# Performance work log

Hardware: AMD Instinct MI355X
Metric: run time of the kernel (lower is better)

The kernel has to match this reference:

```python
import jax, jax.numpy as jnp
import numpy as np

N_NODES = 20000
N_EDGES = 640000
NUM_TYPES = 100
D = 512


def sage_layer(h, src, dst, Ws, Wn, b):
    # DGL SAGEConv(aggregator='mean'): mean over in-neighbors (messages flow src->dst)
    msg = jax.ops.segment_sum(h[src], dst, num_segments=N_NODES)  # [N, d]
    deg = jax.ops.segment_sum(jnp.ones((src.shape[0],), h.dtype), dst, num_segments=N_NODES)
    h_neigh = msg / jnp.maximum(deg, 1.0)[:, None]
    return h @ Ws + h_neigh @ Wn + b


def setup_inputs() -> dict:
    key = jax.random.key(0)
    ks = jax.random.split(key, 10)
    s = 1.0 / np.sqrt(D)
    return {
        "in_feat": jax.random.randint(ks[0], (N_NODES,), 0, NUM_TYPES),
        "src": jax.random.randint(ks[1], (N_EDGES,), 0, N_NODES),
        "dst": jax.random.randint(ks[2], (N_EDGES,), 0, N_NODES),
        "emb": jax.random.normal(ks[3], (NUM_TYPES, D), dtype=jnp.float32),
        "Ws0": jax.random.normal(ks[4], (D, D), dtype=jnp.float32) * s,
        "Wn0": jax.random.normal(ks[5], (D, D), dtype=jnp.float32) * s,
        "b0": jnp.zeros((D,), jnp.float32),
        "Ws1": jax.random.normal(ks[6], (D, D), dtype=jnp.float32) * s,
        "Wn1": jax.random.normal(ks[7], (D, D), dtype=jnp.float32) * s,
        "b1": jnp.zeros((D,), jnp.float32),
    }


def reference(in_feat, src, dst, emb, Ws0, Wn0, b0, Ws1, Wn1, b1):
    h = emb[in_feat]                                   # embedding lookup [N, D]
    h = jax.nn.relu(sage_layer(h, src, dst, Ws0, Wn0, b0))
    h = jax.nn.relu(sage_layer(h, src, dst, Ws1, Wn1, b1))
    return h
```

## Files before the change

### kernel.cpp

```cpp
#include <hip/hip_runtime.h>
#include <hip/hip_bf16.h>
#include <stdint.h>

#define N_NODES 20000
#define N_EDGES 640000
#define DIM     512
#define M_PAD   20096
#define NTYPE   100
#define KEXT    256
#define CSTRIDE 96
#define CURS    16

using bf16 = __hip_bfloat16;
typedef __attribute__((ext_vector_type(4))) float floatx4;
typedef __attribute__((ext_vector_type(2))) float floatx2;
typedef __attribute__((ext_vector_type(8))) short short8;

__device__ __forceinline__ void async16(const void* g, void* l) {
    __builtin_amdgcn_global_load_lds(
        (const __attribute__((address_space(1))) void*)g,
        (__attribute__((address_space(3))) void*)l, 16, 0, 0);
}

__device__ __forceinline__ uint8_t f32_to_fp8(float v) {
    unsigned p = (unsigned)__builtin_amdgcn_cvt_pk_fp8_f32(v, v, 0, false);
    return (uint8_t)(p & 0xffu);
}

__global__ void prep_w_kernel(const float* __restrict__ Ws1, const float* __restrict__ Wn1,
                              bf16* __restrict__ Wt) {
    __shared__ float tile[32][33];
    const int w = blockIdx.z;
    const float* W = (w == 0) ? Ws1 : Wn1;
    const int k0 = blockIdx.x * 32;
    const int n0 = blockIdx.y * 32;
    const int tx = threadIdx.x, ty = threadIdx.y;
#pragma unroll
    for (int i = 0; i < 4; ++i)
        tile[ty + i * 8][tx] = W[(size_t)(k0 + ty + i * 8) * DIM + n0 + tx];
    __syncthreads();
    bf16* O = Wt + (size_t)w * DIM * DIM;
#pragma unroll
    for (int i = 0; i < 4; ++i)
        O[(size_t)(n0 + ty + i * 8) * DIM + k0 + tx] = __float2bfloat16(tile[tx][ty + i * 8]);
}

__global__ void proj_kernel(const float* __restrict__ emb, const float* __restrict__ Ws0,
                            const float* __restrict__ Wn0, bf16* __restrict__ Pb) {
    const int idx = blockIdx.x * 256 + threadIdx.x;
    const int w = blockIdx.y;
    const int t = idx >> 9;
    const int n = idx & 511;
    bf16* dstp = Pb + (size_t)n * KEXT + ((w == 0) ? (128 + t) : t);
    if (t >= NTYPE) { *dstp = __float2bfloat16(0.0f); return; }
    const float* W = (w == 0) ? Ws0 : Wn0;
    const float* erow = emb + (size_t)t * DIM;
    float s = 0.0f;
#pragma unroll 8
    for (int k = 0; k < DIM; ++k) s += erow[k] * W[(size_t)k * DIM + n];
    *dstp = __float2bfloat16(s);
}

__global__ void graph_kernel(const int* __restrict__ src, const int* __restrict__ dst,
                             const int* __restrict__ feat, int* __restrict__ cursor,
                             int* __restrict__ csr) {
    const int e = blockIdx.x * 256 + threadIdx.x;
    if (e < N_EDGES) {
        const int d = dst[e];
        const int s = src[e];
        const int t = feat[s];
        const int p = atomicAdd(&cursor[d * CURS], 1);
        if (p < CSTRIDE) csr[d * CSTRIDE + p] = s | (t << 16);
    }
}

__global__ void normalize_kernel(const int* __restrict__ csr, const int* __restrict__ cursor,
                                 const int* __restrict__ feat, bf16* __restrict__ A0) {
    __shared__ int hist[4 * 128];
    const int tid = threadIdx.x;
    hist[tid] = 0;
    hist[tid + 256] = 0;
    __syncthreads();
    const int wave = tid >> 6, lane = tid & 63;
    const int node = blockIdx.x * 4 + wave;
    int dg = 0;
    if (node < N_NODES) {
        dg = cursor[node * CURS];
        if (dg > CSTRIDE) dg = CSTRIDE;
        for (int l = lane; l < dg; l += 64) {
            const int v = csr[node * CSTRIDE + l];
            atomicAdd(&hist[wave * 128 + (v >> 16)], 1);
        }
    }
    __syncthreads();
    const int c = lane * 4;
    union { uint2 u; bf16 b[4]; } o;
    if (node < N_NODES) {
        if (c < 128) {
            const float inv = 1.0f / (float)(dg > 0 ? dg : 1);
#pragma unroll
            for (int q = 0; q < 4; ++q)
                o.b[q] = __float2bfloat16((float)hist[wave * 128 + c + q] * inv);
        } else {
            const int f = feat[node];
#pragma unroll
            for (int q = 0; q < 4; ++q)
                o.b[q] = __float2bfloat16((c - 128 + q == f) ? 1.0f : 0.0f);
        }
    } else {
#pragma unroll
        for (int q = 0; q < 4; ++q) o.b[q] = __float2bfloat16(0.0f);
    }
    *(uint2*)(A0 + (size_t)node * KEXT + c) = o.u;
}

__global__ void aggregate_kernel(const uint8_t* __restrict__ h8, const int* __restrict__ cursor,
                                 const int* __restrict__ csr, bf16* __restrict__ hn) {
    const int wave = threadIdx.x >> 6;
    const int lane = threadIdx.x & 63;
    const int node = blockIdx.x * 4 + wave;
    const int p = blockIdx.y;
    const int eg = lane >> 3, sc = lane & 7;
    int dg = cursor[node * CURS];
    if (dg > CSTRIDE) dg = CSTRIDE;
    const int base = node * CSTRIDE;
    const int colb = p * 128 + sc * 16;
    float acc[16];
#pragma unroll
    for (int q = 0; q < 16; ++q) acc[q] = 0.0f;

    for (int i = 0; i < dg; i += 8) {
        const int e = i + eg;
        if (e < dg) {
            const int s = csr[base + e] & 0xffff;
            const uint4 r = *(const uint4*)(h8 + (size_t)s * DIM + colb);
            const unsigned v[4] = {r.x, r.y, r.z, r.w};
#pragma unroll
            for (int q = 0; q < 4; ++q) {
                floatx2 lo = __builtin_amdgcn_cvt_pk_f32_fp8((int)v[q], false);
                floatx2 hi = __builtin_amdgcn_cvt_pk_f32_fp8((int)v[q], true);
                acc[4 * q]     += lo.x;
                acc[4 * q + 1] += lo.y;
                acc[4 * q + 2] += hi.x;
                acc[4 * q + 3] += hi.y;
            }
        }
    }
#pragma unroll
    for (int mk = 8; mk <= 32; mk <<= 1)
#pragma unroll
        for (int q = 0; q < 16; ++q) acc[q] += __shfl_xor(acc[q], mk, 64);

    if (eg == 0) {
        const float scale = 1.0f / (float)(dg > 0 ? dg : 1);
        union { uint4 u; bf16 b[8]; } o0, o1;
#pragma unroll
        for (int q = 0; q < 8; ++q) o0.b[q] = __float2bfloat16(acc[q] * scale);
#pragma unroll
        for (int q = 0; q < 8; ++q) o1.b[q] = __float2bfloat16(acc[8 + q] * scale);
        bf16* outp = hn + (size_t)node * DIM + p * 128 + sc * 16;
        *(uint4*)outp = o0.u;
        *(uint4*)(outp + 8) = o1.u;
    }
}

__global__ __launch_bounds__(256)
void gemm0_kernel(const bf16* __restrict__ A0, const bf16* __restrict__ Pb,
                  const float* __restrict__ bias, bf16* __restrict__ h1,
                  uint8_t* __restrict__ h8) {
    const int tid  = threadIdx.x;
    const int lane = tid & 63;
    const int wave = tid >> 6;
    const int wm = wave & 1, wn = wave >> 1;
    const int gn = blockIdx.x, gm = blockIdx.y;
    const int lrow = lane & 15;
    const int kq   = lane >> 4;

    floatx4 acc[4][4] = {};
#pragma unroll
    for (int kk = 0; kk < KEXT; kk += 32) {
        short8 af[4], bfr[4];
#pragma unroll
        for (int i = 0; i < 4; ++i)
            af[i] = *(const short8*)(A0 + (size_t)(gm * 128 + wm * 64 + i * 16 + lrow) * KEXT + kk + kq * 8);
#pragma unroll
        for (int j = 0; j < 4; ++j)
            bfr[j] = *(const short8*)(Pb + (size_t)(gn * 128 + wn * 64 + j * 16 + lrow) * KEXT + kk + kq * 8);
#pragma unroll
        for (int i = 0; i < 4; ++i)
#pragma unroll
            for (int j = 0; j < 4; ++j)
                acc[i][j] = __builtin_amdgcn_mfma_f32_16x16x32_bf16(af[i], bfr[j], acc[i][j], 0, 0, 0);
    }

    const int colInTile = lane & 15;
    const int rquad = lane >> 4;
    float bv[4];
#pragma unroll
    for (int j = 0; j < 4; ++j) bv[j] = bias[gn * 128 + wn * 64 + j * 16 + colInTile];
#pragma unroll
    for (int i = 0; i < 4; ++i) {
#pragma unroll
        for (int r = 0; r < 4; ++r) {
            const int mrow = gm * 128 + wm * 64 + i * 16 + rquad * 4 + r;
            if (mrow >= N_NODES) {
                if (mrow < M_PAD) {
#pragma unroll
                    for (int j = 0; j < 4; ++j) {
                        const int ncol = gn * 128 + wn * 64 + j * 16 + colInTile;
                        h1[(size_t)mrow * DIM + ncol] = __float2bfloat16(0.0f);
                    }
                }
                continue;
            }
#pragma unroll
            for (int j = 0; j < 4; ++j) {
                const int ncol = gn * 128 + wn * 64 + j * 16 + colInTile;
                float v = acc[i][j][r] + bv[j];
                v = v > 0.0f ? v : 0.0f;
                h1[(size_t)mrow * DIM + ncol] = __float2bfloat16(v);
                h8[(size_t)mrow * DIM + ncol] = f32_to_fp8(v);
            }
        }
    }
}

__global__ __launch_bounds__(256)
void gemm1_kernel(const bf16* __restrict__ A, const bf16* __restrict__ Nh,
                  const bf16* __restrict__ Bst, const bf16* __restrict__ Bnt,
                  const float* __restrict__ bias, float* __restrict__ out) {
    __shared__ bf16 As[2][128 * 64];
    __shared__ bf16 Bs[2][128 * 64];
    const int tid  = threadIdx.x;
    const int lane = tid & 63;
    const int wave = tid >> 6;
    const int wm = wave & 1, wn = wave >> 1;
    const int gn = blockIdx.x, gm = blockIdx.y;

    floatx4 acc[4][4] = {};
    const int lrow = lane & 15;
    const int kq   = lane >> 4;

    auto stage = [&](int kt, int buf) {
        const bf16* Ap = (kt < 8) ? A : Nh;
        const bf16* Bp = (kt < 8) ? Bst : Bnt;
        const int k0 = (kt & 7) * 64;
#pragma unroll
        for (int it = 0; it < 4; ++it) {
            const int chunk = tid + it * 256;
            const int row = chunk >> 3;
            const int ch  = (chunk & 7) ^ (row & 7);
            async16(Ap + (size_t)(gm * 128 + row) * DIM + k0 + ch * 8, As[buf] + chunk * 8);
            async16(Bp + (size_t)(gn * 128 + row) * DIM + k0 + ch * 8, Bs[buf] + chunk * 8);
        }
    };

    stage(0, 0);
    __syncthreads();
    for (int kt = 0; kt < 16; ++kt) {
        if (kt + 1 < 16) stage(kt + 1, (kt + 1) & 1);
        const bf16* Asb = As[kt & 1];
        const bf16* Bsb = Bs[kt & 1];
#pragma unroll
        for (int kk8 = 0; kk8 < 8; kk8 += 4) {
            short8 af[4], bfr[4];
#pragma unroll
            for (int i = 0; i < 4; ++i) {
                const int r = wm * 64 + i * 16 + lrow;
                af[i] = *(const short8*)(Asb + (r * 8 + ((kq + kk8) ^ (r & 7))) * 8);
            }
#pragma unroll
            for (int j = 0; j < 4; ++j) {
                const int r = wn * 64 + j * 16 + lrow;
                bfr[j] = *(const short8*)(Bsb + (r * 8 + ((kq + kk8) ^ (r & 7))) * 8);
            }
#pragma unroll
            for (int i = 0; i < 4; ++i)
#pragma unroll
                for (int j = 0; j < 4; ++j)
                    acc[i][j] = __builtin_amdgcn_mfma_f32_16x16x32_bf16(af[i], bfr[j], acc[i][j], 0, 0, 0);
        }
        __syncthreads();
    }

    const int colInTile = lane & 15;
    const int rquad = lane >> 4;
    float bv[4];
#pragma unroll
    for (int j = 0; j < 4; ++j) bv[j] = bias[gn * 128 + wn * 64 + j * 16 + colInTile];
#pragma unroll
    for (int i = 0; i < 4; ++i) {
#pragma unroll
        for (int j = 0; j < 4; ++j) {
            const int ncol = gn * 128 + wn * 64 + j * 16 + colInTile;
#pragma unroll
            for (int r = 0; r < 4; ++r) {
                const int mrow = gm * 128 + wm * 64 + i * 16 + rquad * 4 + r;
                if (mrow < N_NODES) {
                    float v = acc[i][j][r] + bv[j];
                    out[(size_t)mrow * DIM + ncol] = v > 0.0f ? v : 0.0f;
                }
            }
        }
    }
}

extern "C" void kernel_launch(void* const* d_in, const int* in_sizes, int n_in,
                              void* d_out, int out_size, void* d_ws, size_t ws_size,
                              hipStream_t stream) {
    const int*   feat = (const int*)d_in[0];
    const int*   src  = (const int*)d_in[1];
    const int*   dst  = (const int*)d_in[2];
    const float* emb  = (const float*)d_in[3];
    const float* Ws0  = (const float*)d_in[4];
    const float* Wn0  = (const float*)d_in[5];
    const float* b0   = (const float*)d_in[6];
    const float* Ws1  = (const float*)d_in[7];
    const float* Wn1  = (const float*)d_in[8];
    const float* b1   = (const float*)d_in[9];
    float* out = (float*)d_out;

    uint8_t* w = (uint8_t*)d_ws;
    auto alloc = [&](size_t bytes) -> void* {
        void* p = (void*)w;
        w += (bytes + 255) & ~(size_t)255;
        return p;
    };
    bf16*     h1      = (bf16*)alloc((size_t)M_PAD * DIM * 2);
    uint8_t*  h8      = (uint8_t*)alloc((size_t)N_NODES * DIM);
    bf16*     hn      = (bf16*)alloc((size_t)M_PAD * DIM * 2);
    bf16*     Wt      = (bf16*)alloc((size_t)2 * DIM * DIM * 2);
    bf16*     Pb      = (bf16*)alloc((size_t)DIM * KEXT * 2);
    bf16*     A0      = (bf16*)alloc((size_t)M_PAD * KEXT * 2);
    int*      cursor  = (int*)alloc((size_t)N_NODES * CURS * 4);
    int*      csr     = (int*)alloc((size_t)N_NODES * CSTRIDE * 4);

    hipMemsetAsync(cursor, 0, (size_t)N_NODES * CURS * 4, stream);

    prep_w_kernel<<<dim3(16, 16, 2), dim3(32, 8), 0, stream>>>(Ws1, Wn1, Wt);
    proj_kernel<<<dim3(256, 2), 256, 0, stream>>>(emb, Ws0, Wn0, Pb);

    graph_kernel<<<N_EDGES / 256, 256, 0, stream>>>(src, dst, feat, cursor, csr);
    normalize_kernel<<<M_PAD / 4, 256, 0, stream>>>(csr, cursor, feat, A0);

    gemm0_kernel<<<dim3(4, 157), 256, 0, stream>>>(A0, Pb, b0, h1, h8);

    aggregate_kernel<<<dim3(5000, 4), 256, 0, stream>>>(h8, cursor, csr, hn);
    gemm1_kernel<<<dim3(4, 157), 256, 0, stream>>>(
        h1, hn, Wt, Wt + DIM * DIM, b1, out);
}
```

Before: 277.9 us.

## Fuse setup kernels, stage CSR in LDS for aggregation, single-buffer gemm1

```diff
diff --git a/kernel.cpp b/kernel.cpp
--- a/kernel.cpp
+++ b/kernel.cpp
@@ -27,38 +27,50 @@
     return (uint8_t)(p & 0xffu);
 }
 
-__global__ void prep_w_kernel(const float* __restrict__ Ws1, const float* __restrict__ Wn1,
-                              bf16* __restrict__ Wt) {
+__global__ __launch_bounds__(256)
+void setup_kernel(const float* __restrict__ Ws0, const float* __restrict__ Wn0,
+                  const float* __restrict__ Ws1, const float* __restrict__ Wn1,
+                  const float* __restrict__ emb, bf16* __restrict__ Wt,
+                  bf16* __restrict__ Pb, int* __restrict__ cursor) {
     __shared__ float tile[32][33];
-    const int w = blockIdx.z;
-    const float* W = (w == 0) ? Ws1 : Wn1;
-    const int k0 = blockIdx.x * 32;
-    const int n0 = blockIdx.y * 32;
-    const int tx = threadIdx.x, ty = threadIdx.y;
-#pragma unroll
-    for (int i = 0; i < 4; ++i)
-        tile[ty + i * 8][tx] = W[(size_t)(k0 + ty + i * 8) * DIM + n0 + tx];
-    __syncthreads();
-    bf16* O = Wt + (size_t)w * DIM * DIM;
-#pragma unroll
-    for (int i = 0; i < 4; ++i)
-        O[(size_t)(n0 + ty + i * 8) * DIM + k0 + tx] = __float2bfloat16(tile[tx][ty + i * 8]);
-}
-
-__global__ void proj_kernel(const float* __restrict__ emb, const float* __restrict__ Ws0,
-                            const float* __restrict__ Wn0, bf16* __restrict__ Pb) {
-    const int idx = blockIdx.x * 256 + threadIdx.x;
-    const int w = blockIdx.y;
-    const int t = idx >> 9;
-    const int n = idx & 511;
-    bf16* dstp = Pb + (size_t)n * KEXT + ((w == 0) ? (128 + t) : t);
-    if (t >= NTYPE) { *dstp = __float2bfloat16(0.0f); return; }
-    const float* W = (w == 0) ? Ws0 : Wn0;
-    const float* erow = emb + (size_t)t * DIM;
-    float s = 0.0f;
+    const int b = blockIdx.x;
+    const int tid = threadIdx.x;
+    if (b < 512) {
+        const int w = b >> 8;
+        const int rem = b & 255;
+        const int k0 = (rem & 15) * 32;
+        const int n0 = (rem >> 4) * 32;
+        const float* W = (w == 0) ? Ws1 : Wn1;
+        const int tx = tid & 31, ty = tid >> 5;
+#pragma unroll
+        for (int i = 0; i < 4; ++i)
+            tile[ty + i * 8][tx] = W[(size_t)(k0 + ty + i * 8) * DIM + n0 + tx];
+        __syncthreads();
+        bf16* O = Wt + (size_t)w * DIM * DIM;
+#pragma unroll
+        for (int i = 0; i < 4; ++i)
+            O[(size_t)(n0 + ty + i * 8) * DIM + k0 + tx] = __float2bfloat16(tile[tx][ty + i * 8]);
+    } else if (b < 1024) {
+        const int pb = b - 512;
+        const int w = pb >> 8;
+        const int idx = (pb & 255) * 256 + tid;
+        const int t = idx >> 9;
+        const int n = idx & 511;
+        bf16* dstp = Pb + (size_t)n * KEXT + ((w == 0) ? (128 + t) : t);
+        if (t >= NTYPE) { *dstp = __float2bfloat16(0.0f); return; }
+        const float* W = (w == 0) ? Ws0 : Wn0;
+        const float* erow = emb + (size_t)t * DIM;
+        float s = 0.0f;
 #pragma unroll 8
-    for (int k = 0; k < DIM; ++k) s += erow[k] * W[(size_t)k * DIM + n];
-    *dstp = __float2bfloat16(s);
+        for (int k = 0; k < DIM; ++k) s += erow[k] * W[(size_t)k * DIM + n];
+        *dstp = __float2bfloat16(s);
+    } else {
+        const int idx = (b - 1024) * 256 + tid;
+        if (idx < (N_NODES * CURS) / 4) {
+            uint4 z; z.x = 0; z.y = 0; z.z = 0; z.w = 0;
+            ((uint4*)cursor)[idx] = z;
+        }
+    }
 }
 
 __global__ void graph_kernel(const int* __restrict__ src, const int* __restrict__ dst,
@@ -116,49 +128,56 @@
 
 __global__ void aggregate_kernel(const uint8_t* __restrict__ h8, const int* __restrict__ cursor,
                                  const int* __restrict__ csr, bf16* __restrict__ hn) {
-    const int wave = threadIdx.x >> 6;
-    const int lane = threadIdx.x & 63;
-    const int node = blockIdx.x * 4 + wave;
-    const int p = blockIdx.y;
+    __shared__ int scsr[CSTRIDE];
+    __shared__ int sdeg;
+    const int tid = threadIdx.x;
+    const int node = blockIdx.x;
+    if (tid == 0) {
+        int d = cursor[node * CURS];
+        sdeg = (d > CSTRIDE) ? CSTRIDE : d;
+    }
+    if (tid < CSTRIDE) scsr[tid] = csr[node * CSTRIDE + tid];
+    __syncthreads();
+    const int dg = sdeg;
+    const int wave = tid >> 6;
+    const int lane = tid & 63;
     const int eg = lane >> 3, sc = lane & 7;
-    int dg = cursor[node * CURS];
-    if (dg > CSTRIDE) dg = CSTRIDE;
-    const int base = node * CSTRIDE;
-    const int colb = p * 128 + sc * 16;
-    float acc[16];
-#pragma unroll
-    for (int q = 0; q < 16; ++q) acc[q] = 0.0f;
+    const int colb = wave * 128 + sc * 16;
+    floatx2 acc[8] = {};
 
     for (int i = 0; i < dg; i += 8) {
         const int e = i + eg;
         if (e < dg) {
-            const int s = csr[base + e] & 0xffff;
+            const int s = scsr[e] & 0xffff;
             const uint4 r = *(const uint4*)(h8 + (size_t)s * DIM + colb);
             const unsigned v[4] = {r.x, r.y, r.z, r.w};
 #pragma unroll
             for (int q = 0; q < 4; ++q) {
-                floatx2 lo = __builtin_amdgcn_cvt_pk_f32_fp8((int)v[q], false);
-                floatx2 hi = __builtin_amdgcn_cvt_pk_f32_fp8((int)v[q], true);
-                acc[4 * q]     += lo.x;
-                acc[4 * q + 1] += lo.y;
-                acc[4 * q + 2] += hi.x;
-                acc[4 * q + 3] += hi.y;
+                acc[2 * q]     += __builtin_amdgcn_cvt_pk_f32_fp8((int)v[q], false);
+                acc[2 * q + 1] += __builtin_amdgcn_cvt_pk_f32_fp8((int)v[q], true);
             }
         }
     }
 #pragma unroll
     for (int mk = 8; mk <= 32; mk <<= 1)
 #pragma unroll
-        for (int q = 0; q < 16; ++q) acc[q] += __shfl_xor(acc[q], mk, 64);
+        for (int q = 0; q < 8; ++q) {
+            float lo = acc[q][0], hi = acc[q][1];
+            acc[q][0] = lo + __shfl_xor(lo, mk, 64);
+            acc[q][1] = hi + __shfl_xor(hi, mk, 64);
+        }
 
     if (eg == 0) {
         const float scale = 1.0f / (float)(dg > 0 ? dg : 1);
         union { uint4 u; bf16 b[8]; } o0, o1;
 #pragma unroll
-        for (int q = 0; q < 8; ++q) o0.b[q] = __float2bfloat16(acc[q] * scale);
-#pragma unroll
-        for (int q = 0; q < 8; ++q) o1.b[q] = __float2bfloat16(acc[8 + q] * scale);
-        bf16* outp = hn + (size_t)node * DIM + p * 128 + sc * 16;
+        for (int q = 0; q < 4; ++q) {
+            o0.b[2 * q]     = __float2bfloat16(acc[q][0] * scale);
+            o0.b[2 * q + 1] = __float2bfloat16(acc[q][1] * scale);
+            o1.b[2 * q]     = __float2bfloat16(acc[4 + q][0] * scale);
+            o1.b[2 * q + 1] = __float2bfloat16(acc[4 + q][1] * scale);
+        }
+        bf16* outp = hn + (size_t)node * DIM + colb;
         *(uint4*)outp = o0.u;
         *(uint4*)(outp + 8) = o1.u;
     }
@@ -225,12 +244,12 @@
     }
 }
 
-__global__ __launch_bounds__(256)
+__global__ __launch_bounds__(256, 4)
 void gemm1_kernel(const bf16* __restrict__ A, const bf16* __restrict__ Nh,
                   const bf16* __restrict__ Bst, const bf16* __restrict__ Bnt,
                   const float* __restrict__ bias, float* __restrict__ out) {
-    __shared__ bf16 As[2][128 * 64];
-    __shared__ bf16 Bs[2][128 * 64];
+    __shared__ bf16 As[128 * 64];
+    __shared__ bf16 Bs[128 * 64];
     const int tid  = threadIdx.x;
     const int lane = tid & 63;
     const int wave = tid >> 6;
@@ -241,38 +260,32 @@
     const int lrow = lane & 15;
     const int kq   = lane >> 4;
 
-    auto stage = [&](int kt, int buf) {
+    for (int kt = 0; kt < 16; ++kt) {
         const bf16* Ap = (kt < 8) ? A : Nh;
         const bf16* Bp = (kt < 8) ? Bst : Bnt;
         const int k0 = (kt & 7) * 64;
+        __syncthreads();
 #pragma unroll
         for (int it = 0; it < 4; ++it) {
             const int chunk = tid + it * 256;
             const int row = chunk >> 3;
             const int ch  = (chunk & 7) ^ (row & 7);
-            async16(Ap + (size_t)(gm * 128 + row) * DIM + k0 + ch * 8, As[buf] + chunk * 8);
-            async16(Bp + (size_t)(gn * 128 + row) * DIM + k0 + ch * 8, Bs[buf] + chunk * 8);
-        }
-    };
-
-    stage(0, 0);
-    __syncthreads();
-    for (int kt = 0; kt < 16; ++kt) {
-        if (kt + 1 < 16) stage(kt + 1, (kt + 1) & 1);
-        const bf16* Asb = As[kt & 1];
-        const bf16* Bsb = Bs[kt & 1];
+            async16(Ap + (size_t)(gm * 128 + row) * DIM + k0 + ch * 8, As + chunk * 8);
+            async16(Bp + (size_t)(gn * 128 + row) * DIM + k0 + ch * 8, Bs + chunk * 8);
+        }
+        __syncthreads();
 #pragma unroll
         for (int kk8 = 0; kk8 < 8; kk8 += 4) {
             short8 af[4], bfr[4];
 #pragma unroll
             for (int i = 0; i < 4; ++i) {
                 const int r = wm * 64 + i * 16 + lrow;
-                af[i] = *(const short8*)(Asb + (r * 8 + ((kq + kk8) ^ (r & 7))) * 8);
+                af[i] = *(const short8*)(As + (r * 8 + ((kq + kk8) ^ (r & 7))) * 8);
             }
 #pragma unroll
             for (int j = 0; j < 4; ++j) {
                 const int r = wn * 64 + j * 16 + lrow;
-                bfr[j] = *(const short8*)(Bsb + (r * 8 + ((kq + kk8) ^ (r & 7))) * 8);
+                bfr[j] = *(const short8*)(Bs + (r * 8 + ((kq + kk8) ^ (r & 7))) * 8);
             }
 #pragma unroll
             for (int i = 0; i < 4; ++i)
@@ -280,7 +293,6 @@
                 for (int j = 0; j < 4; ++j)
                     acc[i][j] = __builtin_amdgcn_mfma_f32_16x16x32_bf16(af[i], bfr[j], acc[i][j], 0, 0, 0);
         }
-        __syncthreads();
     }
 
     const int colInTile = lane & 15;
@@ -335,17 +347,14 @@
     int*      cursor  = (int*)alloc((size_t)N_NODES * CURS * 4);
     int*      csr     = (int*)alloc((size_t)N_NODES * CSTRIDE * 4);
 
-    hipMemsetAsync(cursor, 0, (size_t)N_NODES * CURS * 4, stream);
-
-    prep_w_kernel<<<dim3(16, 16, 2), dim3(32, 8), 0, stream>>>(Ws1, Wn1, Wt);
-    proj_kernel<<<dim3(256, 2), 256, 0, stream>>>(emb, Ws0, Wn0, Pb);
+    setup_kernel<<<1337, 256, 0, stream>>>(Ws0, Wn0, Ws1, Wn1, emb, Wt, Pb, cursor);
 
     graph_kernel<<<N_EDGES / 256, 256, 0, stream>>>(src, dst, feat, cursor, csr);
     normalize_kernel<<<M_PAD / 4, 256, 0, stream>>>(csr, cursor, feat, A0);
 
     gemm0_kernel<<<dim3(4, 157), 256, 0, stream>>>(A0, Pb, b0, h1, h8);
 
-    aggregate_kernel<<<dim3(5000, 4), 256, 0, stream>>>(h8, cursor, csr, hn);
+    aggregate_kernel<<<N_NODES, 256, 0, stream>>>(h8, cursor, csr, hn);
     gemm1_kernel<<<dim3(4, 157), 256, 0, stream>>>(
         h1, hn, Wt, Wt + DIM * DIM, b1, out);
 }
```

New measurement: 263.3 us. 5.2% less time.
